# Kernel tuning notes

Measured on AMD Instinct MI355X. Metric: run time of the kernel, lower is better.

Reference implementation:

```python
import jax, jax.numpy as jnp
import numpy as np

IO, H, S, N = 64, 1024, 512, 64

def setup_inputs() -> dict:
    key = jax.random.key(0)
    ks = jax.random.split(key, 6)
    scale = 0.05  # keep activations in a sane range for tanh/softmax
    return {
        "states": jax.random.normal(ks[0], (N, S, H), jnp.float32) * scale,
        "output_set": jax.random.normal(ks[1], (IO, H), jnp.float32) * scale,
        "Wo": jax.random.normal(ks[2], (2 * H, H), jnp.float32) * scale,
        "bo": jax.random.normal(ks[3], (H,), jnp.float32) * scale,
        "Wc": jax.random.normal(ks[4], (IO * H, IO), jnp.float32) * scale,
        "bc": jax.random.normal(ks[5], (IO,), jnp.float32) * scale,
    }

def reference(states, output_set, Wo, bo, Wc, bc):
    # Batched over the n_states Python loop of the original module.
    # attn scores: output_set [io,h] x states [n,s,h] -> [n,io,s]
    attn = jnp.einsum('ih,nsh->nis', output_set, states)
    attn = jax.nn.softmax(attn, axis=-1)  # softmax over context (sm_over_context=True)
    mix = jnp.einsum('nis,nsh->nih', attn, states)            # [n,io,h]
    out = jnp.broadcast_to(output_set[None], mix.shape)       # [n,io,h]
    combined = jnp.concatenate([mix, out], axis=-1)           # [n,io,2h]
    o = combined @ Wo + bo                                    # linear_out: 2h -> h
    logits = jnp.tanh(o).reshape(o.shape[0], -1) @ Wc + bc    # C: io*h -> io
    return logits
```

## Files before the change

kernel.cpp:

```cpp
#include <hip/hip_runtime.h>
#include <hip/hip_bf16.h>

#define IOdim 64
#define Hdim  1024
#define Sdim  512
#define Nbat  64

typedef __bf16 bf16x8_t __attribute__((ext_vector_type(8)));
typedef float  f32x4_t  __attribute__((ext_vector_type(4)));

#define MFMA16(a, b, c) __builtin_amdgcn_mfma_f32_16x16x32_bf16((a), (b), (c), 0, 0, 0)

__device__ __forceinline__ unsigned short f2bf(float f) {
    return __builtin_bit_cast(unsigned short, (__bf16)f);
}
__device__ __forceinline__ bf16x8_t cvt8(float4 p0, float4 p1) {
    bf16x8_t b;
    b[0] = (__bf16)p0.x; b[1] = (__bf16)p0.y; b[2] = (__bf16)p0.z; b[3] = (__bf16)p0.w;
    b[4] = (__bf16)p1.x; b[5] = (__bf16)p1.y; b[6] = (__bf16)p1.z; b[7] = (__bf16)p1.w;
    return b;
}
__device__ __forceinline__ void async16(const void* g, void* l) {
    __builtin_amdgcn_global_load_lds(
        (const __attribute__((address_space(1))) void*)g,
        (__attribute__((address_space(3))) void*)l, 16, 0, 0);
}

__global__ __launch_bounds__(256) void cvt_kernel(const float* __restrict__ in,
                                                  unsigned short* __restrict__ outp,
                                                  int nElem) {
    int idx = blockIdx.x * 256 + threadIdx.x;
    if (idx < nElem) outp[idx] = f2bf(in[idx]);
}

__global__ __launch_bounds__(256) void transpose_cvt(const float* __restrict__ in,
                                                     unsigned short* __restrict__ outp,
                                                     int R, int C) {
    __shared__ float tile[32][33];
    int c0 = blockIdx.x * 32, r0 = blockIdx.y * 32;
    int tx = threadIdx.x, ty = threadIdx.y;
#pragma unroll
    for (int i = 0; i < 4; i++) {
        int r = ty + i * 8;
        tile[r][tx] = in[(size_t)(r0 + r) * C + c0 + tx];
    }
    __syncthreads();
#pragma unroll
    for (int i = 0; i < 4; i++) {
        int r = ty + i * 8;
        outp[(size_t)(c0 + r) * R + r0 + tx] = f2bf(tile[tx][r]);
    }
}

__global__ __launch_bounds__(256) void ob_kernel(const unsigned short* __restrict__ osb,
                                                 const unsigned short* __restrict__ woT,
                                                 const float* __restrict__ bo,
                                                 float* __restrict__ ob) {
    int h0 = blockIdx.x * 64;
    int tid = threadIdx.x, lane = tid & 63, w = tid >> 6;
    int col = lane & 15, quad = lane >> 4;
    f32x4_t acc[4] = {};
    const unsigned short* bp  = woT + (size_t)(h0 + w * 16 + col) * 2048 + 1024 + quad * 8;
    const unsigned short* apb = osb + (size_t)col * 1024 + quad * 8;
    for (int kc = 0; kc < 1024; kc += 32) {
        bf16x8_t bfrag = *(const bf16x8_t*)(bp + kc);
#pragma unroll
        for (int a = 0; a < 4; a++) {
            bf16x8_t afrag = *(const bf16x8_t*)(apb + (size_t)a * 16 * 1024 + kc);
            acc[a] = MFMA16(bfrag, afrag, acc[a]);
        }
    }
#pragma unroll
    for (int a = 0; a < 4; a++)
#pragma unroll
        for (int r = 0; r < 4; r++) {
            int i = a * 16 + col;
            int h = h0 + w * 16 + quad * 4 + r;
            ob[(size_t)i * Hdim + h] = acc[a][r] + bo[h];
        }
}

__global__ __launch_bounds__(256) void scores_kernel(const float* __restrict__ states,
                                                     const unsigned short* __restrict__ osb,
                                                     float* __restrict__ attnf) {
    __shared__ float Bst[64 * 64];
    __shared__ unsigned short Ast[64 * 64];
    int n = blockIdx.y, s0 = blockIdx.x * 64;
    int tid = threadIdx.x, lane = tid & 63, w = tid >> 6;
    int col = lane & 15, quad = lane >> 4;
    const float* bsrc = states + ((size_t)(n * Sdim + s0 + (tid >> 4)) << 10)
                      + (((tid & 15) ^ ((tid >> 4) & 7)) << 2);
    const unsigned short* asrc = osb + ((size_t)(tid >> 3) << 10)
                      + (((tid & 7) ^ ((tid >> 3) & 7)) << 3);
    float* bdst = Bst + tid * 4;
    unsigned short* adst = Ast + tid * 8;
    int xs = col & 7;
    f32x4_t acc[4] = {};
    for (int kc = 0; kc < Hdim; kc += 64) {
#pragma unroll
        for (int j = 0; j < 4; j++)
            async16(bsrc + ((size_t)j << 14) + kc, bdst + j * 1024);
#pragma unroll
        for (int j = 0; j < 2; j++)
            async16(asrc + ((size_t)j << 15) + kc, adst + j * 2048);
        __syncthreads();
#pragma unroll
        for (int kk = 0; kk < 2; kk++) {
            int R = w * 16 + col;
            int sg = kk * 8 + quad * 2;
            float4 f0 = *(const float4*)(Bst + R * 64 + ((sg ^ xs) << 2));
            float4 f1 = *(const float4*)(Bst + R * 64 + (((sg + 1) ^ xs) << 2));
            bf16x8_t bfrag = cvt8(f0, f1);
#pragma unroll
            for (int a = 0; a < 4; a++) {
                bf16x8_t afrag = *(const bf16x8_t*)(Ast + (a * 16 + col) * 64
                                                    + (((kk * 4 + quad) ^ xs) << 3));
                acc[a] = MFMA16(afrag, bfrag, acc[a]);
            }
        }
        __syncthreads();
    }
    float* obp = attnf + (size_t)(n * IOdim) * Sdim + s0 + w * 16 + col;
#pragma unroll
    for (int a = 0; a < 4; a++)
#pragma unroll
        for (int r = 0; r < 4; r++) {
            int i = a * 16 + quad * 4 + r;
            obp[(size_t)i * Sdim] = acc[a][r];
        }
}

__global__ __launch_bounds__(256) void softmax_kernel(const float* __restrict__ attnf,
                                                      unsigned short* __restrict__ attnb) {
    int row = blockIdx.x * 4 + (threadIdx.x >> 6);
    int lane = threadIdx.x & 63;
    const float* p = attnf + (size_t)row * Sdim + lane * 8;
    float4 v0 = ((const float4*)p)[0];
    float4 v1 = ((const float4*)p)[1];
    float v[8] = {v0.x, v0.y, v0.z, v0.w, v1.x, v1.y, v1.z, v1.w};
    float m = v[0];
#pragma unroll
    for (int j = 1; j < 8; j++) m = fmaxf(m, v[j]);
#pragma unroll
    for (int off = 32; off > 0; off >>= 1) m = fmaxf(m, __shfl_xor(m, off));
    float sum = 0.f;
#pragma unroll
    for (int j = 0; j < 8; j++) { v[j] = __expf(v[j] - m); sum += v[j]; }
#pragma unroll
    for (int off = 32; off > 0; off >>= 1) sum += __shfl_xor(sum, off);
    float inv = 1.0f / sum;
    union { unsigned short u[8]; uint4 q; } res;
#pragma unroll
    for (int j = 0; j < 8; j++) res.u[j] = f2bf(v[j] * inv);
    *(uint4*)(attnb + (size_t)row * Sdim + lane * 8) = res.q;
}

__global__ __launch_bounds__(256) void mix_kernel(const float* __restrict__ states,
                                                  const unsigned short* __restrict__ attnb,
                                                  unsigned short* __restrict__ mixb) {
    __shared__ unsigned short Tlds[64 * 72];
    int n = blockIdx.y, h0 = blockIdx.x * 64;
    int tid = threadIdx.x, lane = tid & 63, g = tid >> 6;
    int col = lane & 15, quad = lane >> 4;
    f32x4_t acc0 = {0,0,0,0}, acc1 = {0,0,0,0}, acc2 = {0,0,0,0}, acc3 = {0,0,0,0};
    const unsigned short* ap = attnb + (size_t)(n * IOdim + col) * Sdim + quad * 8;
    const float* sbase = states + (size_t)n * Sdim * Hdim + h0 + lane;
    float cur[16];
#pragma unroll
    for (int rep = 0; rep < 16; rep++) cur[rep] = sbase[(size_t)(g * 16 + rep) * Hdim];
    for (int sc = 0; sc < Sdim; sc += 64) {
        union { unsigned short u[16]; uint4 q[2]; } pk;
#pragma unroll
        for (int rep = 0; rep < 16; rep++) pk.u[rep] = f2bf(cur[rep]);
        if (sc) __syncthreads();
        *(uint4*)(Tlds + lane * 72 + g * 16)     = pk.q[0];
        *(uint4*)(Tlds + lane * 72 + g * 16 + 8) = pk.q[1];
        if (sc + 64 < Sdim) {
#pragma unroll
            for (int rep = 0; rep < 16; rep++)
                cur[rep] = sbase[(size_t)(sc + 64 + g * 16 + rep) * Hdim];
        }
        __syncthreads();
#pragma unroll
        for (int ks = 0; ks < 64; ks += 32) {
            bf16x8_t b  = *(const bf16x8_t*)(Tlds + (g * 16 + col) * 72 + ks + quad * 8);
            bf16x8_t a0 = *(const bf16x8_t*)(ap + sc + ks);
            bf16x8_t a1 = *(const bf16x8_t*)(ap + 16 * Sdim + sc + ks);
            bf16x8_t a2 = *(const bf16x8_t*)(ap + 32 * Sdim + sc + ks);
            bf16x8_t a3 = *(const bf16x8_t*)(ap + 48 * Sdim + sc + ks);
            acc0 = MFMA16(a0, b, acc0);
            acc1 = MFMA16(a1, b, acc1);
            acc2 = MFMA16(a2, b, acc2);
            acc3 = MFMA16(a3, b, acc3);
        }
    }
    f32x4_t accs[4] = {acc0, acc1, acc2, acc3};
    int h = h0 + g * 16 + col;
#pragma unroll
    for (int ai = 0; ai < 4; ai++)
#pragma unroll
        for (int r = 0; r < 4; r++) {
            int i = ai * 16 + quad * 4 + r;
            mixb[(size_t)(n * IOdim + i) * Hdim + h] = f2bf(accs[ai][r]);
        }
}

__global__ __launch_bounds__(256) void out_gemm(const unsigned short* __restrict__ mixb,
                                                const unsigned short* __restrict__ woT,
                                                const float* __restrict__ ob,
                                                unsigned short* __restrict__ tb) {
    __shared__ unsigned short Ald[128 * 64];
    __shared__ unsigned short Bld[64 * 64];
    int h0 = blockIdx.x * 64, r0 = blockIdx.y * 128;
    int tid = threadIdx.x, lane = tid & 63, w = tid >> 6;
    int col = lane & 15, quad = lane >> 4;
    int wx = w & 1, wy = w >> 1;
    int sw = ((tid & 7) ^ ((tid >> 3) & 7)) * 8;
    const unsigned short* m1 = mixb + (size_t)(r0 + (tid >> 3)) * Hdim + sw;
    const unsigned short* w1 = woT + (size_t)(h0 + (tid >> 3)) * 2048 + sw;
    unsigned short* lA = Ald + (size_t)tid * 8;
    unsigned short* lB = Bld + (size_t)tid * 8;
    int xs = col & 7;
    f32x4_t acc[4][2] = {};
    for (int kc = 0; kc < 1024; kc += 64) {
#pragma unroll
        for (int j = 0; j < 4; j++)
            async16(m1 + (size_t)j * 32 * Hdim + kc, lA + j * 2048);
#pragma unroll
        for (int j = 0; j < 2; j++)
            async16(w1 + (size_t)j * 32 * 2048 + kc, lB + j * 2048);
        __syncthreads();
#pragma unroll
        for (int kk = 0; kk < 2; kk++) {
            bf16x8_t bfr[2];
#pragma unroll
            for (int ni = 0; ni < 2; ni++)
                bfr[ni] = *(const bf16x8_t*)(Bld + (wx * 32 + ni * 16 + col) * 64
                                             + (((kk * 4 + quad) ^ xs) << 3));
#pragma unroll
            for (int mi = 0; mi < 4; mi++) {
                bf16x8_t af = *(const bf16x8_t*)(Ald + (wy * 64 + mi * 16 + col) * 64
                                                 + (((kk * 4 + quad) ^ xs) << 3));
#pragma unroll
                for (int ni = 0; ni < 2; ni++)
                    acc[mi][ni] = MFMA16(af, bfr[ni], acc[mi][ni]);
            }
        }
        __syncthreads();
    }
#pragma unroll
    for (int ni = 0; ni < 2; ni++) {
        int h = h0 + wx * 32 + ni * 16 + col;
#pragma unroll
        for (int mi = 0; mi < 4; mi++)
#pragma unroll
            for (int r = 0; r < 4; r++) {
                int rr = r0 + wy * 64 + mi * 16 + quad * 4 + r;
                int i = rr & 63;
                tb[(size_t)rr * Hdim + h] = f2bf(tanhf(acc[mi][ni][r] + ob[(size_t)i * Hdim + h]));
            }
    }
}

__global__ __launch_bounds__(256) void final_gemm(const unsigned short* __restrict__ tb,
                                                  const unsigned short* __restrict__ wcT,
                                                  float* __restrict__ partials) {
    int kc0 = blockIdx.x * 128;
    int tid = threadIdx.x, lane = tid & 63, g = tid >> 6;
    int col = lane & 15, quad = lane >> 4;
    f32x4_t acc0 = {0,0,0,0}, acc1 = {0,0,0,0}, acc2 = {0,0,0,0}, acc3 = {0,0,0,0};
    const unsigned short* ap = tb + (size_t)col * 65536 + kc0 + quad * 8;
    const unsigned short* bp = wcT + (size_t)(g * 16 + col) * 65536 + kc0 + quad * 8;
    bf16x8_t B[2], A0[2], A1[2], A2[2], A3[2];
#pragma unroll
    for (int t = 0; t < 2; t++) {
        B[t]  = *(const bf16x8_t*)(bp + t * 32);
        A0[t] = *(const bf16x8_t*)(ap + t * 32);
        A1[t] = *(const bf16x8_t*)(ap + (size_t)16 * 65536 + t * 32);
        A2[t] = *(const bf16x8_t*)(ap + (size_t)32 * 65536 + t * 32);
        A3[t] = *(const bf16x8_t*)(ap + (size_t)48 * 65536 + t * 32);
    }
#pragma unroll
    for (int c = 0; c < 4; c++) {
        int p = c & 1;
        acc0 = MFMA16(A0[p], B[p], acc0);
        acc1 = MFMA16(A1[p], B[p], acc1);
        acc2 = MFMA16(A2[p], B[p], acc2);
        acc3 = MFMA16(A3[p], B[p], acc3);
        if (c + 2 < 4) {
            int kn = (c + 2) * 32;
            B[p]  = *(const bf16x8_t*)(bp + kn);
            A0[p] = *(const bf16x8_t*)(ap + kn);
            A1[p] = *(const bf16x8_t*)(ap + (size_t)16 * 65536 + kn);
            A2[p] = *(const bf16x8_t*)(ap + (size_t)32 * 65536 + kn);
            A3[p] = *(const bf16x8_t*)(ap + (size_t)48 * 65536 + kn);
        }
    }
    f32x4_t accs[4] = {acc0, acc1, acc2, acc3};
    int j = g * 16 + col;
    float* pb = partials + blockIdx.x * 4096;
#pragma unroll
    for (int ai = 0; ai < 4; ai++)
#pragma unroll
        for (int r = 0; r < 4; r++) {
            int nn = ai * 16 + quad * 4 + r;
            pb[nn * 64 + j] = accs[ai][r];
        }
}

__global__ __launch_bounds__(256) void reduce_kernel(const float* __restrict__ partials,
                                                     const float* __restrict__ bc,
                                                     float* __restrict__ out) {
    __shared__ float red[4][64];
    int tid = threadIdx.x, lane = tid & 63, w = tid >> 6;
    int idx = blockIdx.x * 64 + lane;
    float s = 0.f;
#pragma unroll 4
    for (int c = w; c < 512; c += 4) s += partials[(size_t)c * 4096 + idx];
    red[w][lane] = s;
    __syncthreads();
    if (w == 0)
        out[idx] = red[0][lane] + red[1][lane] + red[2][lane] + red[3][lane] + bc[idx & 63];
}

extern "C" void kernel_launch(void* const* d_in, const int* in_sizes, int n_in,
                              void* d_out, int out_size, void* d_ws, size_t ws_size,
                              hipStream_t stream) {
    const float* states     = (const float*)d_in[0];
    const float* output_set = (const float*)d_in[1];
    const float* Wo         = (const float*)d_in[2];
    const float* bo         = (const float*)d_in[3];
    const float* Wc         = (const float*)d_in[4];
    const float* bc         = (const float*)d_in[5];
    float* out = (float*)d_out;

    char* ws = (char*)d_ws;
    float*          attnf = (float*)ws;
    float*          parts = (float*)ws;
    unsigned short* attnb = (unsigned short*)(ws + (8u  << 20));
    unsigned short* mixb  = (unsigned short*)(ws + (12u << 20));
    unsigned short* tb    = (unsigned short*)(ws + (20u << 20));
    unsigned short* woT   = (unsigned short*)(ws + (28u << 20));
    unsigned short* osb   = (unsigned short*)(ws + (32u << 20));
    unsigned short* wcT   = (unsigned short*)(ws + (32u << 20) + (1u << 18));
    float*          obuf  = (float*)(ws + (40u << 20) + (1u << 18));

    cvt_kernel<<<dim3(IOdim * Hdim / 256), dim3(256), 0, stream>>>(output_set, osb, IOdim * Hdim);
    transpose_cvt<<<dim3(Hdim / 32, 2048 / 32), dim3(32, 8), 0, stream>>>(Wo, woT, 2048, Hdim);
    transpose_cvt<<<dim3(64 / 32, 65536 / 32), dim3(32, 8), 0, stream>>>(Wc, wcT, 65536, 64);
    ob_kernel<<<dim3(Hdim / 64), dim3(256), 0, stream>>>(osb, woT, bo, obuf);
    scores_kernel<<<dim3(Sdim / 64, Nbat), dim3(256), 0, stream>>>(states, osb, attnf);
    softmax_kernel<<<dim3(Nbat * IOdim / 4), dim3(256), 0, stream>>>(attnf, attnb);
    mix_kernel<<<dim3(Hdim / 64, Nbat), dim3(256), 0, stream>>>(states, attnb, mixb);
    out_gemm<<<dim3(Hdim / 64, Nbat * IOdim / 128), dim3(256), 0, stream>>>(mixb, woT, obuf, tb);
    final_gemm<<<dim3(512), dim3(256), 0, stream>>>(tb, wcT, parts);
    reduce_kernel<<<dim3(64), dim3(256), 0, stream>>>(parts, bc, out);
}
```

Measured before the change: 334.8 us.

## Double-buffer LDS tiles in scores, mix and out GEMM kernels

Adds ping-pong LDS buffers so the async global-to-LDS loads for the next K tile are issued before the MFMA work on the current tile, with a single waitcnt plus barrier per iteration. In mix_kernel, alternating buffers let one of the two barriers per step be dropped. The goal is to hide global load latency behind compute. In exchange, LDS use per block doubles, which may lower occupancy, and the waitcnt vmcnt(0) still forces the prefetch to finish at the end of every iteration.

```diff
diff --git a/kernel.cpp b/kernel.cpp
--- a/kernel.cpp
+++ b/kernel.cpp
@@ -25,6 +25,10 @@
         (const __attribute__((address_space(1))) void*)g,
         (__attribute__((address_space(3))) void*)l, 16, 0, 0);
 }
+#define PIPE_SYNC() do { \
+    asm volatile("s_waitcnt vmcnt(0)" ::: "memory"); \
+    __builtin_amdgcn_s_barrier(); \
+} while (0)
 
 __global__ __launch_bounds__(256) void cvt_kernel(const float* __restrict__ in,
                                                   unsigned short* __restrict__ outp,
@@ -83,8 +87,8 @@
 __global__ __launch_bounds__(256) void scores_kernel(const float* __restrict__ states,
                                                      const unsigned short* __restrict__ osb,
                                                      float* __restrict__ attnf) {
-    __shared__ float Bst[64 * 64];
-    __shared__ unsigned short Ast[64 * 64];
+    __shared__ float Bst[2][64 * 64];
+    __shared__ unsigned short Ast[2][64 * 64];
     int n = blockIdx.y, s0 = blockIdx.x * 64;
     int tid = threadIdx.x, lane = tid & 63, w = tid >> 6;
     int col = lane & 15, quad = lane >> 4;
@@ -92,34 +96,41 @@
                       + (((tid & 15) ^ ((tid >> 4) & 7)) << 2);
     const unsigned short* asrc = osb + ((size_t)(tid >> 3) << 10)
                       + (((tid & 7) ^ ((tid >> 3) & 7)) << 3);
-    float* bdst = Bst + tid * 4;
-    unsigned short* adst = Ast + tid * 8;
     int xs = col & 7;
+    int R = w * 16 + col;
+    float* B0 = Bst[0]; float* B1 = Bst[1];
+    unsigned short* A0 = Ast[0]; unsigned short* A1 = Ast[1];
     f32x4_t acc[4] = {};
-    for (int kc = 0; kc < Hdim; kc += 64) {
-#pragma unroll
-        for (int j = 0; j < 4; j++)
-            async16(bsrc + ((size_t)j << 14) + kc, bdst + j * 1024);
-#pragma unroll
-        for (int j = 0; j < 2; j++)
-            async16(asrc + ((size_t)j << 15) + kc, adst + j * 2048);
-        __syncthreads();
+
+#define SC_STAGE(kc, Bb, Ab) do { \
+    _Pragma("unroll") for (int j = 0; j < 4; j++) \
+        async16(bsrc + ((size_t)j << 14) + (kc), (Bb) + tid * 4 + j * 1024); \
+    _Pragma("unroll") for (int j = 0; j < 2; j++) \
+        async16(asrc + ((size_t)j << 15) + (kc), (Ab) + tid * 8 + j * 2048); \
+} while (0)
+
+    SC_STAGE(0, B0, A0);
+    PIPE_SYNC();
+    for (int t = 0; t < 16; ++t) {
+        if (t + 1 < 16) SC_STAGE((t + 1) * 64, B1, A1);
 #pragma unroll
         for (int kk = 0; kk < 2; kk++) {
-            int R = w * 16 + col;
             int sg = kk * 8 + quad * 2;
-            float4 f0 = *(const float4*)(Bst + R * 64 + ((sg ^ xs) << 2));
-            float4 f1 = *(const float4*)(Bst + R * 64 + (((sg + 1) ^ xs) << 2));
+            float4 f0 = *(const float4*)(B0 + R * 64 + ((sg ^ xs) << 2));
+            float4 f1 = *(const float4*)(B0 + R * 64 + (((sg + 1) ^ xs) << 2));
             bf16x8_t bfrag = cvt8(f0, f1);
 #pragma unroll
             for (int a = 0; a < 4; a++) {
-                bf16x8_t afrag = *(const bf16x8_t*)(Ast + (a * 16 + col) * 64
+                bf16x8_t afrag = *(const bf16x8_t*)(A0 + (a * 16 + col) * 64
                                                     + (((kk * 4 + quad) ^ xs) << 3));
                 acc[a] = MFMA16(afrag, bfrag, acc[a]);
             }
         }
-        __syncthreads();
-    }
+        PIPE_SYNC();
+        float* tB = B0; B0 = B1; B1 = tB;
+        unsigned short* tA = A0; A0 = A1; A1 = tA;
+    }
+#undef SC_STAGE
     float* obp = attnf + (size_t)(n * IOdim) * Sdim + s0 + w * 16 + col;
 #pragma unroll
     for (int a = 0; a < 4; a++)
@@ -158,7 +169,7 @@
 __global__ __launch_bounds__(256) void mix_kernel(const float* __restrict__ states,
                                                   const unsigned short* __restrict__ attnb,
                                                   unsigned short* __restrict__ mixb) {
-    __shared__ unsigned short Tlds[64 * 72];
+    __shared__ unsigned short Tlds[2][64 * 72];
     int n = blockIdx.y, h0 = blockIdx.x * 64;
     int tid = threadIdx.x, lane = tid & 63, g = tid >> 6;
     int col = lane & 15, quad = lane >> 4;
@@ -168,14 +179,15 @@
     float cur[16];
 #pragma unroll
     for (int rep = 0; rep < 16; rep++) cur[rep] = sbase[(size_t)(g * 16 + rep) * Hdim];
-    for (int sc = 0; sc < Sdim; sc += 64) {
+    for (int t = 0; t < 8; ++t) {
+        int sc = t * 64;
+        unsigned short* Tb = Tlds[t & 1];
         union { unsigned short u[16]; uint4 q[2]; } pk;
 #pragma unroll
         for (int rep = 0; rep < 16; rep++) pk.u[rep] = f2bf(cur[rep]);
-        if (sc) __syncthreads();
-        *(uint4*)(Tlds + lane * 72 + g * 16)     = pk.q[0];
-        *(uint4*)(Tlds + lane * 72 + g * 16 + 8) = pk.q[1];
-        if (sc + 64 < Sdim) {
+        *(uint4*)(Tb + lane * 72 + g * 16)     = pk.q[0];
+        *(uint4*)(Tb + lane * 72 + g * 16 + 8) = pk.q[1];
+        if (t + 1 < 8) {
 #pragma unroll
             for (int rep = 0; rep < 16; rep++)
                 cur[rep] = sbase[(size_t)(sc + 64 + g * 16 + rep) * Hdim];
@@ -183,7 +195,7 @@
         __syncthreads();
 #pragma unroll
         for (int ks = 0; ks < 64; ks += 32) {
-            bf16x8_t b  = *(const bf16x8_t*)(Tlds + (g * 16 + col) * 72 + ks + quad * 8);
+            bf16x8_t b  = *(const bf16x8_t*)(Tb + (g * 16 + col) * 72 + ks + quad * 8);
             bf16x8_t a0 = *(const bf16x8_t*)(ap + sc + ks);
             bf16x8_t a1 = *(const bf16x8_t*)(ap + 16 * Sdim + sc + ks);
             bf16x8_t a2 = *(const bf16x8_t*)(ap + 32 * Sdim + sc + ks);
@@ -209,8 +221,8 @@
                                                 const unsigned short* __restrict__ woT,
                                                 const float* __restrict__ ob,
                                                 unsigned short* __restrict__ tb) {
-    __shared__ unsigned short Ald[128 * 64];
-    __shared__ unsigned short Bld[64 * 64];
+    __shared__ unsigned short Ald[2][128 * 64];
+    __shared__ unsigned short Bld[2][64 * 64];
     int h0 = blockIdx.x * 64, r0 = blockIdx.y * 128;
     int tid = threadIdx.x, lane = tid & 63, w = tid >> 6;
     int col = lane & 15, quad = lane >> 4;
@@ -218,36 +230,44 @@
     int sw = ((tid & 7) ^ ((tid >> 3) & 7)) * 8;
     const unsigned short* m1 = mixb + (size_t)(r0 + (tid >> 3)) * Hdim + sw;
     const unsigned short* w1 = woT + (size_t)(h0 + (tid >> 3)) * 2048 + sw;
-    unsigned short* lA = Ald + (size_t)tid * 8;
-    unsigned short* lB = Bld + (size_t)tid * 8;
     int xs = col & 7;
+    unsigned short* A0 = Ald[0]; unsigned short* A1 = Ald[1];
+    unsigned short* B0 = Bld[0]; unsigned short* B1 = Bld[1];
     f32x4_t acc[4][2] = {};
-    for (int kc = 0; kc < 1024; kc += 64) {
-#pragma unroll
-        for (int j = 0; j < 4; j++)
-            async16(m1 + (size_t)j * 32 * Hdim + kc, lA + j * 2048);
-#pragma unroll
-        for (int j = 0; j < 2; j++)
-            async16(w1 + (size_t)j * 32 * 2048 + kc, lB + j * 2048);
-        __syncthreads();
+
+#define OG_STAGE(kc, Ab, Bb) do { \
+    _Pragma("unroll") for (int j = 0; j < 4; j++) \
+        async16(m1 + (size_t)j * 32 * Hdim + (kc), (Ab) + tid * 8 + j * 2048); \
+    _Pragma("unroll") for (int j = 0; j < 2; j++) \
+        async16(w1 + (size_t)j * 32 * 2048 + (kc), (Bb) + tid * 8 + j * 2048); \
+} while (0)
+
+    OG_STAGE(0, A0, B0);
+    PIPE_SYNC();
+    for (int t = 0; t < 16; ++t) {
+        if (t + 1 < 16) OG_STAGE((t + 1) * 64, A1, B1);
 #pragma unroll
         for (int kk = 0; kk < 2; kk++) {
             bf16x8_t bfr[2];
 #pragma unroll
             for (int ni = 0; ni < 2; ni++)
-                bfr[ni] = *(const bf16x8_t*)(Bld + (wx * 32 + ni * 16 + col) * 64
+                bfr[ni] = *(const bf16x8_t*)(B0 + (wx * 32 + ni * 16 + col) * 64
                                              + (((kk * 4 + quad) ^ xs) << 3));
 #pragma unroll
             for (int mi = 0; mi < 4; mi++) {
-                bf16x8_t af = *(const bf16x8_t*)(Ald + (wy * 64 + mi * 16 + col) * 64
+                bf16x8_t af = *(const bf16x8_t*)(A0 + (wy * 64 + mi * 16 + col) * 64
                                                  + (((kk * 4 + quad) ^ xs) << 3));
 #pragma unroll
                 for (int ni = 0; ni < 2; ni++)
                     acc[mi][ni] = MFMA16(af, bfr[ni], acc[mi][ni]);
             }
         }
-        __syncthreads();
-    }
+        PIPE_SYNC();
+        unsigned short* tp;
+        tp = A0; A0 = A1; A1 = tp;
+        tp = B0; B0 = B1; B1 = tp;
+    }
+#undef OG_STAGE
 #pragma unroll
     for (int ni = 0; ni < 2; ni++) {
         int h = h0 + wx * 32 + ni * 16 + col;
```

Result: faster. 327.5 us (-2.2%).
